# Kernel optimization log

Measured on AMD Instinct MI355X. Metric: run time of the kernel, lower is better.

## Reference

```python
import jax, jax.numpy as jnp
import numpy as np
import math
from itertools import combinations_with_replacement

NDIM = 3
DEGREE = 1
N_CENTERS = 4096
N_QUERY = 65536
S_OUT = 64
EPSILON = 1.0  # scale-invariant kernel (thin_plate_spline) -> epsilon = 1.0


def monomial_powers(ndim, degree):
    """Powers for each monomial of a polynomial (matches torch monomial_powers)."""
    nmonos = math.comb(degree + ndim, ndim)
    out = np.zeros((nmonos, ndim), dtype=np.int32)
    count = 0
    for deg in range(degree + 1):
        for mono in combinations_with_replacement(range(ndim), deg):
            for var in mono:
                out[count, var] += 1
            count += 1
    return out


def setup_inputs() -> dict:
    key = jax.random.key(0)
    k1, k2, k3 = jax.random.split(key, 3)
    r = math.comb(DEGREE + NDIM, NDIM)  # = 4 monomials
    x = jax.random.normal(k1, (N_QUERY, NDIM), dtype=jnp.float32)
    y = jax.random.normal(k2, (N_CENTERS, NDIM), dtype=jnp.float32)
    # coeffs would normally come from torch.linalg.solve on the (n+r, n+r) system;
    # random values exercise the identical forward math.
    coeffs = jax.random.normal(k3, (N_CENTERS + r, S_OUT), dtype=jnp.float32) * 0.1
    shift = jnp.zeros((NDIM,), dtype=jnp.float32)
    scale = jnp.ones((NDIM,), dtype=jnp.float32)
    powers = jnp.asarray(monomial_powers(NDIM, DEGREE))  # (r, ndim) int32
    return {"x": x, "y": y, "coeffs": coeffs, "shift": shift, "scale": scale,
            "powers": powers}


def _tps_kernel_from_sqdist(r2):
    # thin_plate_spline: f(r) = r^2 * log(r) = 0.5 * r2 * log(r2), with f(0) = 0
    safe = jnp.where(r2 > 0, r2, 1.0)
    return jnp.where(r2 > 0, 0.5 * r2 * jnp.log(safe), 0.0)


def reference(x, y, coeffs, shift, scale, powers):
    p = y.shape[0]
    xeps = x * EPSILON            # (nx, d)
    yeps = y * EPSILON            # (p, d)
    # squared pairwise distances without materializing (nx, p, d)
    x2 = jnp.sum(xeps * xeps, axis=1, keepdims=True)        # (nx, 1)
    y2 = jnp.sum(yeps * yeps, axis=1)                        # (p,)
    r2 = jnp.maximum(x2 + y2[None, :] - 2.0 * xeps @ yeps.T, 0.0)  # (nx, p)
    kv = _tps_kernel_from_sqdist(r2)                         # kernel_vector, (nx, p)
    xhat = (x - shift) / scale                               # (nx, d)
    # polynomial_matrix: prod over dims of xhat ** powers -> (nx, r)
    pmat = jnp.prod(xhat[:, None, :] ** powers[None, :, :], axis=-1)
    # [kv | pmat] @ coeffs, split to avoid concat
    return kv @ coeffs[:p] + pmat @ coeffs[p:]
```

## Files before the change

### kernel.cpp

```cpp
#include <hip/hip_runtime.h>

#define NQ   65536
#define NC   4096
#define SOUT 64
#define NR   4
#define KTOT (NC + 64)
#define BM   64
#define NCH  (NC / 64)
#define BP_BLOCKS 130
#define YE_BLOCKS 17

typedef float    f32x4 __attribute__((ext_vector_type(4)));
typedef _Float16 f16x8 __attribute__((ext_vector_type(8)));
typedef __fp16   h16x2 __attribute__((ext_vector_type(2)));
typedef unsigned uint4v __attribute__((ext_vector_type(4)));

__global__ void prep_all(const float* __restrict__ coeffs,
                         const float* __restrict__ y,
                         _Float16* __restrict__ bp,
                         _Float16* __restrict__ ye) {
    if (blockIdx.x < BP_BLOCKS) {
        const int idx = blockIdx.x * 256 + threadIdx.x;
        if (idx >= 65 * 4 * 2 * 64) return;
        const int l  = idx & 63;
        const int kk = (idx >> 6) & 1;
        const int nf = (idx >> 7) & 3;
        const int ch = idx >> 9;
        const int n  = nf * 16 + (l & 15);
        const int ks = ch * 64 + kk * 32 + (l >> 4) * 8;
        f16x8 v;
        #pragma unroll
        for (int j = 0; j < 8; ++j) {
            const int k = ks + j;
            float f = 0.0f;
            if (k < NC)           f = coeffs[(size_t)k * SOUT + n] * 0.34657359f;
            else if (k < NC + NR) f = coeffs[(size_t)k * SOUT + n];
            v[j] = (_Float16)f;
        }
        *(f16x8*)(bp + (size_t)idx * 8) = v;
    } else {
        const int k = (blockIdx.x - BP_BLOCKS) * 256 + threadIdx.x;
        if (k >= KTOT) return;
        f16x8 r = {};
        if (k < NC) {
            const float a = y[k * 3 + 0], b = y[k * 3 + 1], c = y[k * 3 + 2];
            r[0] = (_Float16)(-2.0f * a); r[1] = (_Float16)(-2.0f * b);
            r[2] = (_Float16)(-2.0f * c); r[3] = (_Float16)1.0f;
            r[4] = (_Float16)(a * a + b * b + c * c + 0.02f);
        }
        *(f16x8*)(ye + (size_t)k * 8) = r;
    }
}

__launch_bounds__(256, 4)
__global__ void rbf_mfma18(const float* __restrict__ x,
                           const _Float16* __restrict__ ye,
                           const float* __restrict__ shift,
                           const float* __restrict__ scale,
                           const _Float16* __restrict__ bp,
                           float* __restrict__ out) {
    __shared__ float red[2][32 * 64];

    const int t    = threadIdx.x;
    const int wave = t >> 6;
    const int lane = t & 63;
    const int l15  = lane & 15;
    const int lg   = lane >> 4;
    const int qg   = wave & 1;
    const int kh   = wave >> 1;
    const int qb   = blockIdx.x * BM + qg * 32;
    const int s    = kh * 32;

    f16x8 xef[2];
    uint2  poly01[2];
    #pragma unroll
    for (int qh = 0; qh < 2; ++qh) {
        const int q = qb + qh * 16 + l15;
        const float a = x[q * 3 + 0], b = x[q * 3 + 1], c = x[q * 3 + 2];
        f16x8 v = {};
        if (lg == 0) {
            v[0] = (_Float16)a; v[1] = (_Float16)b; v[2] = (_Float16)c;
            v[3] = (_Float16)(a * a + b * b + c * c); v[4] = (_Float16)1.0f;
        }
        xef[qh] = v;
        h16x2 p0 = __builtin_amdgcn_cvt_pkrtz(1.0f, (a - shift[0]) / scale[0]);
        h16x2 p1 = __builtin_amdgcn_cvt_pkrtz((b - shift[1]) / scale[1],
                                              (c - shift[2]) / scale[2]);
        poly01[qh].x = __builtin_bit_cast(unsigned, p0);
        poly01[qh].y = __builtin_bit_cast(unsigned, p1);
    }

    const _Float16* yp = ye + ((size_t)((l15 >> 2) * 8 + (l15 & 3))) * 8
                            + (size_t)s * 512;
    const _Float16* b0 = bp + (size_t)lane * 8 + (size_t)s * 4096;
    const _Float16* b2 = b0 + 2048;
    const _Float16* bpl = bp + (size_t)lane * 8;

    f32x4 acc[2][4] = {};

    for (int ch = 0; ch < 32; ++ch) {
        f16x8 Y[4];
        Y[0] = *(const f16x8*)(yp + 0);
        Y[1] = *(const f16x8*)(yp + 256);
        Y[2] = *(const f16x8*)(yp + 32);
        Y[3] = *(const f16x8*)(yp + 288);

        f16x8 B[4][2];
        B[0][0] = *(const f16x8*)(b0 + 0);
        B[0][1] = *(const f16x8*)(b0 + 512);
        B[1][0] = *(const f16x8*)(b0 + 1024);
        B[1][1] = *(const f16x8*)(b0 + 1536);
        B[2][0] = *(const f16x8*)(b2 + 0);
        B[2][1] = *(const f16x8*)(b2 + 512);
        B[3][0] = *(const f16x8*)(b2 + 1024);
        B[3][1] = *(const f16x8*)(b2 + 1536);

        yp += 512; b0 += 4096; b2 += 4096;

        #pragma unroll
        for (int qh = 0; qh < 2; ++qh) {
            uint2 w[4];
            #pragma unroll
            for (int kt = 0; kt < 4; ++kt) {
                f32x4 z = {};
                const f32x4 r2 = __builtin_amdgcn_mfma_f32_16x16x32_f16(
                    Y[kt], xef[qh], z, 0, 0, 0);
                float f[4];
                #pragma unroll
                for (int r = 0; r < 4; ++r) {
                    f[r] = r2[r] * __log2f(__builtin_fabsf(r2[r]));
                }
                h16x2 h0 = __builtin_amdgcn_cvt_pkrtz(f[0], f[1]);
                h16x2 h1 = __builtin_amdgcn_cvt_pkrtz(f[2], f[3]);
                w[kt].x = __builtin_bit_cast(unsigned, h0);
                w[kt].y = __builtin_bit_cast(unsigned, h1);
            }
            const uint4v a0 = {w[0].x, w[0].y, w[2].x, w[2].y};
            const uint4v a1 = {w[1].x, w[1].y, w[3].x, w[3].y};
            const f16x8 af0 = __builtin_bit_cast(f16x8, a0);
            const f16x8 af1 = __builtin_bit_cast(f16x8, a1);
            #pragma unroll
            for (int nf = 0; nf < 4; ++nf) {
                acc[qh][nf] = __builtin_amdgcn_mfma_f32_16x16x32_f16(
                    af0, B[nf][0], acc[qh][nf], 0, 0, 0);
                acc[qh][nf] = __builtin_amdgcn_mfma_f32_16x16x32_f16(
                    af1, B[nf][1], acc[qh][nf], 0, 0, 0);
            }
        }
    }

    if (kh == 1) {
        #pragma unroll
        for (int qh = 0; qh < 2; ++qh) {
            uint4v ap = {};
            if (lg == 0) { ap.x = poly01[qh].x; ap.y = poly01[qh].y; }
            const f16x8 afp = __builtin_bit_cast(f16x8, ap);
            #pragma unroll
            for (int nf = 0; nf < 4; ++nf) {
                const f16x8 bpf = *(const f16x8*)(
                    bpl + ((size_t)((NCH * 4 + nf) * 2) << 9));
                acc[qh][nf] = __builtin_amdgcn_mfma_f32_16x16x32_f16(
                    afp, bpf, acc[qh][nf], 0, 0, 0);
            }
        }
        #pragma unroll
        for (int qh = 0; qh < 2; ++qh)
            #pragma unroll
            for (int nf = 0; nf < 4; ++nf)
                #pragma unroll
                for (int r = 0; r < 4; ++r)
                    red[qg][(qh * 16 + nf * 4 + r) * 64 + lane] = acc[qh][nf][r];
    }
    __syncthreads();
    if (kh == 0) {
        #pragma unroll
        for (int qh = 0; qh < 2; ++qh)
            #pragma unroll
            for (int nf = 0; nf < 4; ++nf)
                #pragma unroll
                for (int r = 0; r < 4; ++r)
                    acc[qh][nf][r] += red[qg][(qh * 16 + nf * 4 + r) * 64 + lane];

        #pragma unroll
        for (int qh = 0; qh < 2; ++qh)
            #pragma unroll
            for (int nf = 0; nf < 4; ++nf)
                #pragma unroll
                for (int r = 0; r < 4; ++r)
                    out[(size_t)(qb + qh * 16 + lg * 4 + r) * SOUT + nf * 16 + l15] =
                        acc[qh][nf][r];
    }
}

__launch_bounds__(256)
__global__ void rbf_tps_fallback(const float* __restrict__ x,
                                 const float* __restrict__ y,
                                 const float* __restrict__ coeffs,
                                 const float* __restrict__ shift,
                                 const float* __restrict__ scale,
                                 float* __restrict__ out) {
    __shared__ float4 ytile[NC];
    const int tid = threadIdx.x;
    for (int j = tid; j < NC; j += 256) {
        const float a = y[j * 3], b = y[j * 3 + 1], c = y[j * 3 + 2];
        ytile[j] = make_float4(a, b, c, a * a + b * b + c * c);
    }
    __syncthreads();
    const int q = blockIdx.x * 256 + tid;
    const float x0 = x[q * 3], x1 = x[q * 3 + 1], x2 = x[q * 3 + 2];
    const float xsq = x0 * x0 + x1 * x1 + x2 * x2;
    const float xh0 = (x0 - shift[0]) / scale[0];
    const float xh1 = (x1 - shift[1]) / scale[1];
    const float xh2 = (x2 - shift[2]) / scale[2];
    float acc[SOUT];
    {
        const float* c0 = &coeffs[(size_t)(NC + 0) * SOUT];
        const float* c1 = &coeffs[(size_t)(NC + 1) * SOUT];
        const float* c2 = &coeffs[(size_t)(NC + 2) * SOUT];
        const float* c3 = &coeffs[(size_t)(NC + 3) * SOUT];
        #pragma unroll
        for (int s = 0; s < SOUT; ++s)
            acc[s] = c0[s] + xh0 * c1[s] + xh1 * c2[s] + xh2 * c3[s];
    }
    #pragma unroll 2
    for (int j = 0; j < NC; ++j) {
        const float4 yj = ytile[j];
        const float dot = x0 * yj.x + x1 * yj.y + x2 * yj.z;
        float r2 = fmaf(-2.0f, dot, xsq + yj.w);
        r2 = fmaxf(r2, 0.0f);
        const float f = 0.5f * r2 * __logf(fmaxf(r2, 1e-37f));
        const float* __restrict__ cj = &coeffs[(size_t)j * SOUT];
        #pragma unroll
        for (int s = 0; s < SOUT; ++s) acc[s] = fmaf(f, cj[s], acc[s]);
    }
    float4* o4 = (float4*)&out[(size_t)q * SOUT];
    #pragma unroll
    for (int s = 0; s < SOUT / 4; ++s)
        o4[s] = make_float4(acc[4 * s], acc[4 * s + 1], acc[4 * s + 2], acc[4 * s + 3]);
}

extern "C" void kernel_launch(void* const* d_in, const int* in_sizes, int n_in,
                              void* d_out, int out_size, void* d_ws, size_t ws_size,
                              hipStream_t stream) {
    const float* x      = (const float*)d_in[0];
    const float* y      = (const float*)d_in[1];
    const float* coeffs = (const float*)d_in[2];
    const float* shift  = (const float*)d_in[3];
    const float* scale  = (const float*)d_in[4];
    float* out = (float*)d_out;

    const size_t bp_bytes = (size_t)65 * 4 * 2 * 64 * 8 * sizeof(_Float16);
    const size_t ye_bytes = (size_t)KTOT * 8 * sizeof(_Float16);

    if (ws_size >= bp_bytes + ye_bytes) {
        _Float16* bpw = (_Float16*)d_ws;
        _Float16* yep = (_Float16*)((char*)d_ws + bp_bytes);
        hipLaunchKernelGGL(prep_all, dim3(BP_BLOCKS + YE_BLOCKS), dim3(256),
                           0, stream, coeffs, y, bpw, yep);
        hipLaunchKernelGGL(rbf_mfma18, dim3(NQ / BM), dim3(256), 0, stream,
                           x, yep, shift, scale, bpw, out);
    } else {
        hipLaunchKernelGGL(rbf_tps_fallback, dim3(NQ / 256), dim3(256),
                           0, stream, x, y, coeffs, shift, scale, out);
    }
}
```

Baseline: 67.28 us.

## Software-pipeline kernel-fragment computation against output MFMAs across chunks

Restructures the main loop so each iteration issues the output-accumulation MFMAs for the previous chunk's fragments while computing the log-kernel fragments for the current chunk, with loads for the next chunk issued first. The aim is to interleave the transcendental VALU work with the independent MFMA chain and hide global load latency. It also drops the occupancy hint of 4 blocks per CU from the launch bounds, letting the compiler use more registers for the extra live fragments at the risk of lower occupancy.

```diff
diff --git a/kernel.cpp b/kernel.cpp
--- a/kernel.cpp
+++ b/kernel.cpp
@@ -52,8 +52,8 @@
     }
 }
 
-__launch_bounds__(256, 4)
-__global__ void rbf_mfma18(const float* __restrict__ x,
+__launch_bounds__(256)
+__global__ void rbf_mfma19(const float* __restrict__ x,
                            const _Float16* __restrict__ ye,
                            const float* __restrict__ shift,
                            const float* __restrict__ scale,
@@ -97,70 +97,100 @@
     const _Float16* bpl = bp + (size_t)lane * 8;
 
     f32x4 acc[2][4] = {};
-
-    for (int ch = 0; ch < 32; ++ch) {
-        f16x8 Y[4];
-        Y[0] = *(const f16x8*)(yp + 0);
-        Y[1] = *(const f16x8*)(yp + 256);
-        Y[2] = *(const f16x8*)(yp + 32);
-        Y[3] = *(const f16x8*)(yp + 288);
-
-        f16x8 B[4][2];
-        B[0][0] = *(const f16x8*)(b0 + 0);
-        B[0][1] = *(const f16x8*)(b0 + 512);
-        B[1][0] = *(const f16x8*)(b0 + 1024);
-        B[1][1] = *(const f16x8*)(b0 + 1536);
-        B[2][0] = *(const f16x8*)(b2 + 0);
-        B[2][1] = *(const f16x8*)(b2 + 512);
-        B[3][0] = *(const f16x8*)(b2 + 1024);
-        B[3][1] = *(const f16x8*)(b2 + 1536);
-
-        yp += 512; b0 += 4096; b2 += 4096;
-
-        #pragma unroll
-        for (int qh = 0; qh < 2; ++qh) {
-            uint2 w[4];
-            #pragma unroll
-            for (int kt = 0; kt < 4; ++kt) {
-                f32x4 z = {};
-                const f32x4 r2 = __builtin_amdgcn_mfma_f32_16x16x32_f16(
-                    Y[kt], xef[qh], z, 0, 0, 0);
-                float f[4];
-                #pragma unroll
-                for (int r = 0; r < 4; ++r) {
-                    f[r] = r2[r] * __log2f(__builtin_fabsf(r2[r]));
-                }
-                h16x2 h0 = __builtin_amdgcn_cvt_pkrtz(f[0], f[1]);
-                h16x2 h1 = __builtin_amdgcn_cvt_pkrtz(f[2], f[3]);
-                w[kt].x = __builtin_bit_cast(unsigned, h0);
-                w[kt].y = __builtin_bit_cast(unsigned, h1);
-            }
-            const uint4v a0 = {w[0].x, w[0].y, w[2].x, w[2].y};
-            const uint4v a1 = {w[1].x, w[1].y, w[3].x, w[3].y};
-            const f16x8 af0 = __builtin_bit_cast(f16x8, a0);
-            const f16x8 af1 = __builtin_bit_cast(f16x8, a1);
-            #pragma unroll
-            for (int nf = 0; nf < 4; ++nf) {
-                acc[qh][nf] = __builtin_amdgcn_mfma_f32_16x16x32_f16(
-                    af0, B[nf][0], acc[qh][nf], 0, 0, 0);
-                acc[qh][nf] = __builtin_amdgcn_mfma_f32_16x16x32_f16(
-                    af1, B[nf][1], acc[qh][nf], 0, 0, 0);
-            }
-        }
-    }
+    f16x8 afp[2][2];
+    f16x8 Bp[4][2];
+
+#define LOADC(Y, Bc)                                                          \
+    do {                                                                      \
+        Y[0] = *(const f16x8*)(yp + 0);    Y[1] = *(const f16x8*)(yp + 256);  \
+        Y[2] = *(const f16x8*)(yp + 32);   Y[3] = *(const f16x8*)(yp + 288);  \
+        Bc[0][0] = *(const f16x8*)(b0 + 0);                                   \
+        Bc[0][1] = *(const f16x8*)(b0 + 512);                                 \
+        Bc[1][0] = *(const f16x8*)(b0 + 1024);                                \
+        Bc[1][1] = *(const f16x8*)(b0 + 1536);                                \
+        Bc[2][0] = *(const f16x8*)(b2 + 0);                                   \
+        Bc[2][1] = *(const f16x8*)(b2 + 512);                                 \
+        Bc[3][0] = *(const f16x8*)(b2 + 1024);                                \
+        Bc[3][1] = *(const f16x8*)(b2 + 1536);                                \
+        yp += 512; b0 += 4096; b2 += 4096;                                    \
+    } while (0)
+
+#define FRAGS(Y, af)                                                          \
+    do {                                                                      \
+        _Pragma("unroll")                                                     \
+        for (int qh = 0; qh < 2; ++qh) {                                      \
+            uint2 w[4];                                                       \
+            _Pragma("unroll")                                                 \
+            for (int kt = 0; kt < 4; ++kt) {                                  \
+                f32x4 z = {};                                                 \
+                const f32x4 r2 = __builtin_amdgcn_mfma_f32_16x16x32_f16(      \
+                    Y[kt], xef[qh], z, 0, 0, 0);                              \
+                float f[4];                                                   \
+                _Pragma("unroll")                                             \
+                for (int r = 0; r < 4; ++r)                                   \
+                    f[r] = r2[r] * __log2f(__builtin_fabsf(r2[r]));           \
+                h16x2 h0 = __builtin_amdgcn_cvt_pkrtz(f[0], f[1]);            \
+                h16x2 h1 = __builtin_amdgcn_cvt_pkrtz(f[2], f[3]);            \
+                w[kt].x = __builtin_bit_cast(unsigned, h0);                   \
+                w[kt].y = __builtin_bit_cast(unsigned, h1);                   \
+            }                                                                 \
+            const uint4v a0 = {w[0].x, w[0].y, w[2].x, w[2].y};               \
+            const uint4v a1 = {w[1].x, w[1].y, w[3].x, w[3].y};               \
+            af[qh][0] = __builtin_bit_cast(f16x8, a0);                        \
+            af[qh][1] = __builtin_bit_cast(f16x8, a1);                        \
+        }                                                                     \
+    } while (0)
+
+#define OUTM(af, Bq)                                                          \
+    do {                                                                      \
+        _Pragma("unroll")                                                     \
+        for (int qh = 0; qh < 2; ++qh)                                        \
+            _Pragma("unroll")                                                 \
+            for (int nf = 0; nf < 4; ++nf) {                                  \
+                acc[qh][nf] = __builtin_amdgcn_mfma_f32_16x16x32_f16(         \
+                    af[qh][0], Bq[nf][0], acc[qh][nf], 0, 0, 0);              \
+                acc[qh][nf] = __builtin_amdgcn_mfma_f32_16x16x32_f16(         \
+                    af[qh][1], Bq[nf][1], acc[qh][nf], 0, 0, 0);              \
+            }                                                                 \
+    } while (0)
+
+    {
+        f16x8 Y[4], Bc[4][2];
+        LOADC(Y, Bc);
+        FRAGS(Y, afp);
+        #pragma unroll
+        for (int nf = 0; nf < 4; ++nf) {
+            Bp[nf][0] = Bc[nf][0]; Bp[nf][1] = Bc[nf][1];
+        }
+    }
+    for (int ch = 1; ch < 32; ++ch) {
+        f16x8 Y[4], Bc[4][2];
+        LOADC(Y, Bc);
+        OUTM(afp, Bp);
+        FRAGS(Y, afp);
+        #pragma unroll
+        for (int nf = 0; nf < 4; ++nf) {
+            Bp[nf][0] = Bc[nf][0]; Bp[nf][1] = Bc[nf][1];
+        }
+    }
+    OUTM(afp, Bp);
+
+#undef LOADC
+#undef FRAGS
+#undef OUTM
 
     if (kh == 1) {
         #pragma unroll
         for (int qh = 0; qh < 2; ++qh) {
             uint4v ap = {};
             if (lg == 0) { ap.x = poly01[qh].x; ap.y = poly01[qh].y; }
-            const f16x8 afp = __builtin_bit_cast(f16x8, ap);
+            const f16x8 afq = __builtin_bit_cast(f16x8, ap);
             #pragma unroll
             for (int nf = 0; nf < 4; ++nf) {
                 const f16x8 bpf = *(const f16x8*)(
                     bpl + ((size_t)((NCH * 4 + nf) * 2) << 9));
                 acc[qh][nf] = __builtin_amdgcn_mfma_f32_16x16x32_f16(
-                    afp, bpf, acc[qh][nf], 0, 0, 0);
+                    afq, bpf, acc[qh][nf], 0, 0, 0);
             }
         }
         #pragma unroll
@@ -257,7 +287,7 @@
         _Float16* yep = (_Float16*)((char*)d_ws + bp_bytes);
         hipLaunchKernelGGL(prep_all, dim3(BP_BLOCKS + YE_BLOCKS), dim3(256),
                            0, stream, coeffs, y, bpw, yep);
-        hipLaunchKernelGGL(rbf_mfma18, dim3(NQ / BM), dim3(256), 0, stream,
+        hipLaunchKernelGGL(rbf_mfma19, dim3(NQ / BM), dim3(256), 0, stream,
                            x, yep, shift, scale, bpw, out);
     } else {
         hipLaunchKernelGGL(rbf_tps_fallback, dim3(NQ / 256), dim3(256),
```

After: 82.96 us. +23.3%, slower.
